# Kernel tuning notes

Hardware: AMD Instinct MI355X
Metric: run time of the kernel (lower is better)

## Reference

```python
import jax, jax.numpy as jnp
import numpy as np
from jax.ops import segment_sum

N, E, G, D, L = 50000, 800000, 1024, 300, 5
FEAT = 256
EPS = 1e-5


def setup_inputs() -> dict:
    key = jax.random.key(0)
    ks = jax.random.split(key, 20)
    x = jax.random.randint(ks[0], (N, 2), 0, 3)
    edge_index = jax.random.randint(ks[1], (2, E), 0, N)
    edge_attr = jax.random.randint(ks[2], (E, 2), 0, 3)
    batch = jnp.sort(jax.random.randint(ks[3], (N,), 0, G))
    s = 0.05
    x_emb1 = jax.random.normal(ks[4], (119, D), jnp.float32) * s
    x_emb2 = jax.random.normal(ks[5], (3, D), jnp.float32) * s
    W = jax.random.normal(ks[6], (L, D, D), jnp.float32) * (1.0 / np.sqrt(D))
    b = jnp.zeros((L, D), jnp.float32)
    e1 = jax.random.normal(ks[7], (L, 5, 1), jnp.float32) * s
    e2 = jax.random.normal(ks[8], (L, 3, 1), jnp.float32) * s
    gamma = jnp.ones((L, D), jnp.float32)
    beta = jnp.zeros((L, D), jnp.float32)
    feat_w = jax.random.normal(ks[9], (D, FEAT), jnp.float32) * (1.0 / np.sqrt(D))
    feat_b = jnp.zeros((FEAT,), jnp.float32)
    w1 = jax.random.normal(ks[10], (FEAT, FEAT), jnp.float32) * (1.0 / np.sqrt(FEAT))
    b1 = jnp.zeros((FEAT,), jnp.float32)
    w2 = jax.random.normal(ks[11], (FEAT, FEAT // 2), jnp.float32) * (1.0 / np.sqrt(FEAT))
    b2 = jnp.zeros((FEAT // 2,), jnp.float32)
    return dict(x=x, edge_index=edge_index, edge_attr=edge_attr, batch=batch,
                x_emb1=x_emb1, x_emb2=x_emb2, W=W, b=b, e1=e1, e2=e2,
                gamma=gamma, beta=beta, feat_w=feat_w, feat_b=feat_b,
                w1=w1, b1=b1, w2=w2, b2=b2)


def reference(x, edge_index, edge_attr, batch, x_emb1, x_emb2, W, b, e1, e2,
              gamma, beta, feat_w, feat_b, w1, b1, w2, b2):
    row, col = edge_index[0], edge_index[1]
    # node embedding: atom type + chirality
    h = x_emb1[x[:, 0]] + x_emb2[x[:, 1]]  # [N,D]
    for l in range(L):
        hw = h @ W[l]  # [N,D]
        # scalar edge embedding per edge (emb dim is 1 in the source)
        eemb = e1[l, edge_attr[:, 0], 0] + e2[l, edge_attr[:, 1], 0]  # [E]
        msg = hw[row] + eemb[:, None]  # [E,D]
        agg = segment_sum(msg, col, num_segments=N)
        # self loops: edge_attr = (4, 0)
        self_e = e1[l, 4, 0] + e2[l, 0, 0]
        h = agg + hw + self_e + b[l]
        # BatchNorm1d over nodes (batch statistics, biased var)
        mu = jnp.mean(h, axis=0)
        var = jnp.mean((h - mu) ** 2, axis=0)
        h = (h - mu) * jax.lax.rsqrt(var + EPS) * gamma[l] + beta[l]
        if l < L - 1:
            h = jax.nn.relu(h)
    # global mean pool per graph
    sums = segment_sum(h, batch, num_segments=G)  # [G,D]
    cnt = segment_sum(jnp.ones((h.shape[0],), h.dtype), batch, num_segments=G)
    hg = sums / jnp.maximum(cnt, 1.0)[:, None]
    h_feat = hg @ feat_w + feat_b  # [G,FEAT]
    out = jax.nn.relu(h_feat @ w1 + b1) @ w2 + b2  # [G,FEAT//2]
    return (h_feat, out)
```

## Files before the change

### kernel.cpp

```cpp
#include <hip/hip_runtime.h>
#include <hip/hip_bf16.h>

#define NN 50000
#define EE 800000
#define GG 1024
#define DD 300
#define DP 320
#define LL 5
#define FEAT 256

#define AGGB 6272

typedef __bf16 bf16x8 __attribute__((ext_vector_type(8)));
typedef float  f32x4  __attribute__((ext_vector_type(4)));

#define AS1 __attribute__((address_space(1)))
#define AS3 __attribute__((address_space(3)))

__device__ __forceinline__ void dma16(const __hip_bfloat16* g, __hip_bfloat16* l) {
    auto gp = reinterpret_cast<const AS1 char*>(reinterpret_cast<uintptr_t>(g));
    auto lp = reinterpret_cast<AS3 char*>((unsigned int)(uintptr_t)l);
    __builtin_amdgcn_global_load_lds(gp, lp, 16, 0, 0);
}

__device__ __forceinline__ void addbf8(float* a, int4 q) {
    unsigned int u;
    u = (unsigned int)q.x;
    a[0] += __uint_as_float(u << 16); a[1] += __uint_as_float(u & 0xFFFF0000u);
    u = (unsigned int)q.y;
    a[2] += __uint_as_float(u << 16); a[3] += __uint_as_float(u & 0xFFFF0000u);
    u = (unsigned int)q.z;
    a[4] += __uint_as_float(u << 16); a[5] += __uint_as_float(u & 0xFFFF0000u);
    u = (unsigned int)q.w;
    a[6] += __uint_as_float(u << 16); a[7] += __uint_as_float(u & 0xFFFF0000u);
}

__global__ void embed_kernel(const int* __restrict__ x,
                             const float* __restrict__ emb1,
                             const float* __restrict__ emb2,
                             __hip_bfloat16* __restrict__ A) {
    int idx = blockIdx.x * 256 + threadIdx.x;
    int v = idx / DP, d = idx % DP;
    float val = 0.f;
    if (d < DD) {
        int i0 = x[v * 2 + 0], i1 = x[v * 2 + 1];
        val = emb1[i0 * DD + d] + emb2[i1 * DD + d];
    }
    A[idx] = __float2bfloat16(val);
}

__global__ void hist_kernel(const int* __restrict__ ei, int* __restrict__ deg) {
    int e = blockIdx.x * 256 + threadIdx.x;
    atomicAdd(&deg[ei[EE + e]], 1);
}

__global__ void scan1_kernel(const int* __restrict__ deg, int* __restrict__ ptr,
                             int* __restrict__ bsum) {
    __shared__ int buf[256];
    int tid = threadIdx.x;
    int i = blockIdx.x * 256 + tid;
    int v = (i < NN) ? deg[i] : 0;
    buf[tid] = v; __syncthreads();
    for (int off = 1; off < 256; off <<= 1) {
        int t = (tid >= off) ? buf[tid - off] : 0;
        __syncthreads();
        buf[tid] += t;
        __syncthreads();
    }
    if (i < NN) ptr[i + 1] = buf[tid];
    if (tid == 255) bsum[blockIdx.x] = buf[255];
}

__global__ void scan2_kernel(int* __restrict__ bsum) {
    __shared__ int buf[256];
    int tid = threadIdx.x;
    int v = (tid < 196) ? bsum[tid] : 0;
    buf[tid] = v; __syncthreads();
    for (int off = 1; off < 256; off <<= 1) {
        int t = (tid >= off) ? buf[tid - off] : 0;
        __syncthreads();
        buf[tid] += t;
        __syncthreads();
    }
    if (tid < 196) bsum[tid] = buf[tid] - v;
}

__global__ void scan3_kernel(int* __restrict__ ptr, const int* __restrict__ bsum) {
    int i = blockIdx.x * 256 + threadIdx.x;
    if (i < NN) ptr[i + 1] += bsum[blockIdx.x];
    if (i == 0) ptr[0] = 0;
}

__global__ void scatter_kernel(const int* __restrict__ ei, const int* __restrict__ ea,
                               const int* __restrict__ ptr, int* __restrict__ cur,
                               int* __restrict__ srcout) {
    int e = blockIdx.x * 256 + threadIdx.x;
    int r = ei[e], c = ei[EE + e];
    int a0 = ea[e * 2 + 0], a1 = ea[e * 2 + 1];
    int pos = ptr[c] + atomicAdd(&cur[c], 1);
    srcout[pos] = r | (a0 << 16) | (a1 << 18);
}

__global__ void sv_kernel(const int* __restrict__ ptr, const int* __restrict__ src,
                          const float* __restrict__ e1, const float* __restrict__ e2,
                          float* __restrict__ SV) {
    int v = blockIdx.x * 256 + threadIdx.x;
    if (v >= NN) return;
    float c00 = 0.f, c01 = 0.f, c02 = 0.f, c10 = 0.f, c11 = 0.f, c12 = 0.f;
    int beg = ptr[v], end = ptr[v + 1];
    for (int i = beg; i < end; ++i) {
        int p = src[i];
        int e0 = (p >> 16) & 3, ev = (p >> 18) & 3;
        c00 += (e0 == 0); c01 += (e0 == 1); c02 += (e0 == 2);
        c10 += (ev == 0); c11 += (ev == 1); c12 += (ev == 2);
    }
#pragma unroll
    for (int l = 0; l < LL; ++l) {
        float s = c00 * e1[l * 5 + 0] + c01 * e1[l * 5 + 1] + c02 * e1[l * 5 + 2]
                + c10 * e2[l * 3 + 0] + c11 * e2[l * 3 + 1] + c12 * e2[l * 3 + 2];
        SV[l * NN + v] = s;
    }
}

__global__ void repack_kernel(const float* __restrict__ W,
                              __hip_bfloat16* __restrict__ WT) {
    int idx = blockIdx.x * 256 + threadIdx.x;
    int l = idx / (DP * DP);
    int r = idx - l * DP * DP;
    int ntile = r / 51200; r -= ntile * 51200;
    int ktile = r / 10240; r -= ktile * 10240;
    int nn = r >> 6; r &= 63;
    int pu = r >> 3; int e = r & 7;
    int u = pu ^ (nn & 7);
    int n = ntile * 160 + nn;
    int k = ktile * 64 + u * 8 + e;
    float v = 0.f;
    if (n < DD && k < DD) v = W[l * DD * DD + k * DD + n];
    WT[idx] = __float2bfloat16(v);
}

__global__ __launch_bounds__(256) void gemm_kernel(
        const __hip_bfloat16* __restrict__ A, const __hip_bfloat16* __restrict__ BT,
        __hip_bfloat16* __restrict__ C, int M,
        const float* __restrict__ scale, const float* __restrict__ shift, int fold) {
    __shared__ __align__(16) char smem[38912];
    __hip_bfloat16* As = reinterpret_cast<__hip_bfloat16*>(smem);
    __hip_bfloat16* Bs = reinterpret_cast<__hip_bfloat16*>(smem + 18432);
    __hip_bfloat16* Cs = reinterpret_cast<__hip_bfloat16*>(smem);
    int tid = threadIdx.x;
    int m0 = blockIdx.x * 128;
    int wave = tid >> 6, lane = tid & 63;
    int wm = (wave >> 1) * 64, wn = (wave & 1) * 80;
    int fm = lane & 15, fu = lane >> 4;

    f32x4 acc[4][5];
#pragma unroll
    for (int i = 0; i < 4; ++i)
#pragma unroll
        for (int j = 0; j < 5; ++j) acc[i][j] = (f32x4){0.f, 0.f, 0.f, 0.f};

    const __hip_bfloat16* btile0 = BT + (size_t)blockIdx.y * 51200;

    for (int k0 = 0; k0 < DP; k0 += 64) {
        __syncthreads();
        const __hip_bfloat16* bt = btile0 + (k0 >> 6) * 10240;
#pragma unroll
        for (int i = 0; i < 5; ++i)
            dma16(bt + (size_t)(tid + i * 256) * 8, Bs + (tid + i * 256) * 8);
#pragma unroll
        for (int u = tid; u < 1024; u += 256) {
            int r = u >> 3, p = u & 7;
            int gr = m0 + r;
            int4 val = make_int4(0, 0, 0, 0);
            if (gr < M) {
                val = *reinterpret_cast<const int4*>(A + (size_t)gr * DP + k0 + p * 8);
                if (fold) {
                    __hip_bfloat16* hh = reinterpret_cast<__hip_bfloat16*>(&val);
                    int kb = k0 + p * 8;
#pragma unroll
                    for (int j = 0; j < 8; ++j) {
                        float f = fmaf(__bfloat162float(hh[j]), scale[kb + j], shift[kb + j]);
                        hh[j] = __float2bfloat16(fmaxf(f, 0.f));
                    }
                }
            }
            *reinterpret_cast<int4*>(As + r * 72 + p * 8) = val;
        }
        __syncthreads();
#pragma unroll
        for (int h = 0; h < 2; ++h) {
            bf16x8 af[4], bfr[5];
#pragma unroll
            for (int mt = 0; mt < 4; ++mt)
                af[mt] = *reinterpret_cast<const bf16x8*>(
                    As + (wm + mt * 16 + fm) * 72 + h * 32 + fu * 8);
#pragma unroll
            for (int nt = 0; nt < 5; ++nt) {
                int n = wn + nt * 16 + fm;
                int pu = (h * 4 + fu) ^ (n & 7);
                bfr[nt] = *reinterpret_cast<const bf16x8*>(Bs + n * 64 + pu * 8);
            }
#pragma unroll
            for (int mt = 0; mt < 4; ++mt)
#pragma unroll
                for (int nt = 0; nt < 5; ++nt)
                    acc[mt][nt] = __builtin_amdgcn_mfma_f32_16x16x32_bf16(
                        af[mt], bfr[nt], acc[mt][nt], 0, 0, 0);
        }
    }
    int n0 = blockIdx.y * 160;
    int cc = lane & 15, cr = (lane >> 4) * 4;
#pragma unroll
    for (int h = 0; h < 2; ++h) {
        __syncthreads();
        if ((wave >> 1) == h) {
#pragma unroll
            for (int mt = 0; mt < 4; ++mt)
#pragma unroll
                for (int nt = 0; nt < 5; ++nt)
#pragma unroll
                    for (int r = 0; r < 4; ++r)
                        Cs[(mt * 16 + cr + r) * 168 + wn + nt * 16 + cc] =
                            __float2bfloat16(acc[mt][nt][r]);
        }
        __syncthreads();
#pragma unroll
        for (int u = tid; u < 1280; u += 256) {
            int r = u / 20, c16 = u % 20;
            int row = m0 + h * 64 + r;
            if (row < M)
                *reinterpret_cast<int4*>(C + (size_t)row * DP + n0 + c16 * 8) =
                    *reinterpret_cast<const int4*>(Cs + r * 168 + c16 * 8);
        }
    }
}

__global__ __launch_bounds__(256) void agg_kernel(
        const __hip_bfloat16* __restrict__ HW,
        const int* __restrict__ ptr, const int* __restrict__ src,
        const float* __restrict__ SVl, __hip_bfloat16* __restrict__ AH,
        float* __restrict__ part) {
    int w = threadIdx.x >> 6;
    int lane = threadIdx.x & 63;
    float sx = 0.f, sy = 0.f, sz = 0.f, sw = 0.f, st = 0.f;
    float qx = 0.f, qy = 0.f, qz = 0.f, qw = 0.f, qt = 0.f;

#pragma unroll
    for (int k = 0; k < 2; ++k) {
        int v = blockIdx.x * 8 + w * 2 + k;
        if (v >= NN) break;
        int beg = ptr[v], end = ptr[v + 1];
        const __hip_bfloat16* rv = HW + (size_t)v * DP;
        ushort4 qs = *reinterpret_cast<const ushort4*>(rv + 4 * lane);
        unsigned int ts = reinterpret_cast<const unsigned short*>(rv)[256 + lane];
        float A0x = __uint_as_float((unsigned int)qs.x << 16);
        float A0y = __uint_as_float((unsigned int)qs.y << 16);
        float A0z = __uint_as_float((unsigned int)qs.z << 16);
        float A0w = __uint_as_float((unsigned int)qs.w << 16);
        float A0t = __uint_as_float(ts << 16);
        float A1x = 0.f, A1y = 0.f, A1z = 0.f, A1w = 0.f, A1t = 0.f;
        float A2x = 0.f, A2y = 0.f, A2z = 0.f, A2w = 0.f, A2t = 0.f;
        float A3x = 0.f, A3y = 0.f, A3z = 0.f, A3w = 0.f, A3t = 0.f;
        int i = beg;
        for (; i < end && (i & 3); ++i) {
            int s0 = src[i] & 0xFFFF;
            const __hip_bfloat16* r0 = HW + (size_t)s0 * DP;
            ushort4 q0 = *reinterpret_cast<const ushort4*>(r0 + 4 * lane);
            unsigned int t0 = reinterpret_cast<const unsigned short*>(r0)[256 + lane];
            A0x += __uint_as_float((unsigned int)q0.x << 16);
            A0y += __uint_as_float((unsigned int)q0.y << 16);
            A0z += __uint_as_float((unsigned int)q0.z << 16);
            A0w += __uint_as_float((unsigned int)q0.w << 16);
            A0t += __uint_as_float(t0 << 16);
        }
        for (; i + 4 <= end; i += 4) {
            int4 s4 = *reinterpret_cast<const int4*>(src + i);
            int s0 = s4.x & 0xFFFF, s1 = s4.y & 0xFFFF;
            int s2 = s4.z & 0xFFFF, s3 = s4.w & 0xFFFF;
            const __hip_bfloat16* r0 = HW + (size_t)s0 * DP;
            const __hip_bfloat16* r1 = HW + (size_t)s1 * DP;
            const __hip_bfloat16* r2 = HW + (size_t)s2 * DP;
            const __hip_bfloat16* r3 = HW + (size_t)s3 * DP;
            ushort4 q0 = *reinterpret_cast<const ushort4*>(r0 + 4 * lane);
            ushort4 q1 = *reinterpret_cast<const ushort4*>(r1 + 4 * lane);
            ushort4 q2 = *reinterpret_cast<const ushort4*>(r2 + 4 * lane);
            ushort4 q3 = *reinterpret_cast<const ushort4*>(r3 + 4 * lane);
            unsigned int t0 = reinterpret_cast<const unsigned short*>(r0)[256 + lane];
            unsigned int t1 = reinterpret_cast<const unsigned short*>(r1)[256 + lane];
            unsigned int t2 = reinterpret_cast<const unsigned short*>(r2)[256 + lane];
            unsigned int t3 = reinterpret_cast<const unsigned short*>(r3)[256 + lane];
            A0x += __uint_as_float((unsigned int)q0.x << 16);
            A0y += __uint_as_float((unsigned int)q0.y << 16);
            A0z += __uint_as_float((unsigned int)q0.z << 16);
            A0w += __uint_as_float((unsigned int)q0.w << 16);
            A0t += __uint_as_float(t0 << 16);
            A1x += __uint_as_float((unsigned int)q1.x << 16);
            A1y += __uint_as_float((unsigned int)q1.y << 16);
            A1z += __uint_as_float((unsigned int)q1.z << 16);
            A1w += __uint_as_float((unsigned int)q1.w << 16);
            A1t += __uint_as_float(t1 << 16);
            A2x += __uint_as_float((unsigned int)q2.x << 16);
            A2y += __uint_as_float((unsigned int)q2.y << 16);
            A2z += __uint_as_float((unsigned int)q2.z << 16);
            A2w += __uint_as_float((unsigned int)q2.w << 16);
            A2t += __uint_as_float(t2 << 16);
            A3x += __uint_as_float((unsigned int)q3.x << 16);
            A3y += __uint_as_float((unsigned int)q3.y << 16);
            A3z += __uint_as_float((unsigned int)q3.z << 16);
            A3w += __uint_as_float((unsigned int)q3.w << 16);
            A3t += __uint_as_float(t3 << 16);
        }
        for (; i < end; ++i) {
            int s0 = src[i] & 0xFFFF;
            const __hip_bfloat16* r0 = HW + (size_t)s0 * DP;
            ushort4 q0 = *reinterpret_cast<const ushort4*>(r0 + 4 * lane);
            unsigned int t0 = reinterpret_cast<const unsigned short*>(r0)[256 + lane];
            A0x += __uint_as_float((unsigned int)q0.x << 16);
            A0y += __uint_as_float((unsigned int)q0.y << 16);
            A0z += __uint_as_float((unsigned int)q0.z << 16);
            A0w += __uint_as_float((unsigned int)q0.w << 16);
            A0t += __uint_as_float(t0 << 16);
        }
        float sv = SVl[v];
        float rx = A0x + A1x + A2x + A3x + sv;
        float ry = A0y + A1y + A2y + A3y + sv;
        float rz = A0z + A1z + A2z + A3z + sv;
        float rw = A0w + A1w + A2w + A3w + sv;
        float rt = A0t + A1t + A2t + A3t + sv;
        sx += rx; qx = fmaf(rx, rx, qx);
        sy += ry; qy = fmaf(ry, ry, qy);
        sz += rz; qz = fmaf(rz, rz, qz);
        sw += rw; qw = fmaf(rw, rw, qw);
        st += rt; qt = fmaf(rt, rt, qt);
        __hip_bfloat16* out = AH + (size_t)v * DP;
        union { ushort4 u; __hip_bfloat16 h[4]; } o;
        o.h[0] = __float2bfloat16(rx); o.h[1] = __float2bfloat16(ry);
        o.h[2] = __float2bfloat16(rz); o.h[3] = __float2bfloat16(rw);
        *reinterpret_cast<ushort4*>(out + 4 * lane) = o.u;
        out[256 + lane] = __float2bfloat16(lane < 44 ? rt : 0.f);
    }
    __shared__ float red[4 * 640];
    float* rw_ = red + w * 640;
    rw_[4 * lane + 0] = sx; rw_[4 * lane + 1] = sy;
    rw_[4 * lane + 2] = sz; rw_[4 * lane + 3] = sw;
    rw_[256 + lane] = (lane < 44) ? st : 0.f;
    rw_[320 + 4 * lane + 0] = qx; rw_[320 + 4 * lane + 1] = qy;
    rw_[320 + 4 * lane + 2] = qz; rw_[320 + 4 * lane + 3] = qw;
    rw_[320 + 256 + lane] = (lane < 44) ? qt : 0.f;
    __syncthreads();
    for (int i = threadIdx.x; i < 640; i += 256)
        part[(size_t)blockIdx.x * 640 + i] =
            red[i] + red[640 + i] + red[1280 + i] + red[1920 + i];
}

__global__ void finalize1_kernel(const float* __restrict__ part, float* __restrict__ part2) {
    int b = blockIdx.x;
    const int K = AGGB / 64;
    for (int i = threadIdx.x; i < 640; i += 256) {
        float acc = 0.f;
        for (int k = 0; k < K; ++k)
            acc += part[(size_t)(b * K + k) * 640 + i];
        part2[b * 640 + i] = acc;
    }
}

__global__ void finalize_kernel(const float* __restrict__ part2,
                                const float* __restrict__ gamma_l,
                                const float* __restrict__ beta_l,
                                float* __restrict__ scale, float* __restrict__ shift) {
    int d = threadIdx.x;
    float sc = 0.f, sh = 0.f;
    if (d < DD) {
        float s = 0.f, q = 0.f;
        for (int b = 0; b < 64; ++b) {
            s += part2[b * 640 + d];
            q += part2[b * 640 + 320 + d];
        }
        const float invN = 1.0f / (float)NN;
        float mean = s * invN;
        float var = q * invN - mean * mean;
        var = fmaxf(var, 0.f);
        float rs = rsqrtf(var + 1e-5f);
        sc = rs * gamma_l[d];
        sh = beta_l[d] - mean * sc;
    }
    scale[d] = sc;
    shift[d] = sh;
}

__device__ __forceinline__ int lower_bound_dev(const int* b, int n, int key) {
    int lo = 0, hi = n;
    while (lo < hi) { int mid = (lo + hi) >> 1; if (b[mid] < key) lo = mid + 1; else hi = mid; }
    return lo;
}

__global__ void pool_kernel(const __hip_bfloat16* __restrict__ A, const int* __restrict__ batch,
                            const float* __restrict__ scale, const float* __restrict__ shift,
                            float* __restrict__ HG) {
    int g = blockIdx.x * 4 + (threadIdx.x >> 6);
    int lane = threadIdx.x & 63;
    bool act = lane < 40;
    int lo = lower_bound_dev(batch, NN, g);
    int hi = lower_bound_dev(batch, NN, g + 1);
    const int4 z4 = make_int4(0, 0, 0, 0);
    float a[8];
#pragma unroll
    for (int j = 0; j < 8; ++j) a[j] = 0.f;
    for (int v = lo; v < hi; ++v) {
        int4 q = act ? *reinterpret_cast<const int4*>(A + (size_t)v * DP + 8 * lane) : z4;
        addbf8(a, q);
    }
    if (act) {
        int cnt = hi - lo;
        float inv = 1.0f / (float)(cnt > 0 ? cnt : 1);
        float* out = HG + (size_t)g * DP;
#pragma unroll
        for (int j = 0; j < 8; ++j) {
            int d = 8 * lane + j;
            out[d] = fmaf(a[j] * inv, scale[d], shift[d]);
        }
    }
}

__global__ void feat_kernel(const float* __restrict__ HG,
                            const float* __restrict__ fw,
                            const float* __restrict__ fb,
                            float* __restrict__ HFEAT, float* __restrict__ out0) {
    __shared__ float hgs[DD];
    int g = blockIdx.x, tid = threadIdx.x;
    for (int i = tid; i < DD; i += 256) hgs[i] = HG[(size_t)g * DP + i];
    __syncthreads();
    float acc = fb[tid];
#pragma unroll 4
    for (int k = 0; k < DD; ++k)
        acc = fmaf(hgs[k], fw[k * FEAT + tid], acc);
    HFEAT[g * FEAT + tid] = acc;
    out0[g * FEAT + tid] = acc;
}

__global__ void mlp_kernel(const float* __restrict__ HFEAT,
                           const float* __restrict__ w1, const float* __restrict__ b1,
                           const float* __restrict__ w2, const float* __restrict__ b2,
                           float* __restrict__ out1) {
    __shared__ float hf[FEAT], t[FEAT];
    int g = blockIdx.x, tid = threadIdx.x;
    hf[tid] = HFEAT[g * FEAT + tid];
    __syncthreads();
    float acc = b1[tid];
#pragma unroll 4
    for (int k = 0; k < FEAT; ++k)
        acc = fmaf(hf[k], w1[k * FEAT + tid], acc);
    t[tid] = fmaxf(acc, 0.f);
    __syncthreads();
    if (tid < FEAT / 2) {
        float acc2 = b2[tid];
#pragma unroll 4
        for (int k = 0; k < FEAT; ++k)
            acc2 = fmaf(t[k], w2[k * (FEAT / 2) + tid], acc2);
        out1[g * (FEAT / 2) + tid] = acc2;
    }
}

extern "C" void kernel_launch(void* const* d_in, const int* in_sizes, int n_in,
                              void* d_out, int out_size, void* d_ws, size_t ws_size,
                              hipStream_t stream) {
    const int* x     = (const int*)d_in[0];
    const int* ei    = (const int*)d_in[1];
    const int* ea    = (const int*)d_in[2];
    const int* batch = (const int*)d_in[3];
    const float* emb1  = (const float*)d_in[4];
    const float* emb2  = (const float*)d_in[5];
    const float* W     = (const float*)d_in[6];
    const float* e1    = (const float*)d_in[8];
    const float* e2    = (const float*)d_in[9];
    const float* gamma = (const float*)d_in[10];
    const float* beta  = (const float*)d_in[11];
    const float* fw    = (const float*)d_in[12];
    const float* fb    = (const float*)d_in[13];
    const float* w1    = (const float*)d_in[14];
    const float* b1    = (const float*)d_in[15];
    const float* w2    = (const float*)d_in[16];
    const float* b2    = (const float*)d_in[17];

    char* base = (char*)d_ws;
    size_t off = 0;
    auto carve = [&](size_t bytes) -> void* {
        void* p = base + off;
        off = (off + bytes + 255) & ~(size_t)255;
        return p;
    };
    int*            PTR   = (int*)carve((size_t)(NN + 1) * 4);
    int*            CUR   = (int*)carve((size_t)NN * 4);
    int*            SRC   = (int*)carve((size_t)EE * 4);
    float*          SV    = (float*)carve((size_t)LL * NN * 4);
    int*            BSUM  = (int*)carve(256 * 4);
    float*          PART  = (float*)carve((size_t)AGGB * 640 * 4);
    float*          PART2 = (float*)carve((size_t)64 * 640 * 4);
    float*          SCALE = (float*)carve(DP * 4);
    float*          SHIFT = (float*)carve(DP * 4);
    float*          HG    = (float*)carve((size_t)GG * DP * 4);
    float*          HFEAT = (float*)carve((size_t)GG * FEAT * 4);
    __hip_bfloat16* WT    = (__hip_bfloat16*)carve((size_t)LL * DP * DP * 2);
    __hip_bfloat16* AH    = (__hip_bfloat16*)carve((size_t)NN * DP * 2);
    __hip_bfloat16* HWb   = (__hip_bfloat16*)carve((size_t)NN * DP * 2);

    float* out0 = (float*)d_out;
    float* out1 = (float*)d_out + GG * FEAT;

    hipMemsetAsync(CUR, 0, (size_t)NN * 4, stream);
    embed_kernel<<<(NN * DP) / 256, 256, 0, stream>>>(x, emb1, emb2, AH);
    hist_kernel<<<EE / 256, 256, 0, stream>>>(ei, CUR);
    scan1_kernel<<<196, 256, 0, stream>>>(CUR, PTR, BSUM);
    scan2_kernel<<<1, 256, 0, stream>>>(BSUM);
    scan3_kernel<<<196, 256, 0, stream>>>(PTR, BSUM);
    hipMemsetAsync(CUR, 0, (size_t)NN * 4, stream);
    scatter_kernel<<<EE / 256, 256, 0, stream>>>(ei, ea, PTR, CUR, SRC);
    sv_kernel<<<196, 256, 0, stream>>>(PTR, SRC, e1, e2, SV);
    repack_kernel<<<(LL * DP * DP) / 256, 256, 0, stream>>>(W, WT);

    for (int l = 0; l < LL; ++l) {
        gemm_kernel<<<dim3(391, 2), 256, 0, stream>>>(AH, WT + (size_t)l * DP * DP, HWb, NN,
                                                      SCALE, SHIFT, l > 0 ? 1 : 0);
        agg_kernel<<<AGGB, 256, 0, stream>>>(HWb, PTR, SRC, SV + (size_t)l * NN, AH, PART);
        finalize1_kernel<<<64, 256, 0, stream>>>(PART, PART2);
        finalize_kernel<<<1, 320, 0, stream>>>(PART2, gamma + l * DD, beta + l * DD, SCALE, SHIFT);
    }

    pool_kernel<<<GG / 4, 256, 0, stream>>>(AH, batch, SCALE, SHIFT, HG);
    feat_kernel<<<GG, 256, 0, stream>>>(HG, fw, fb, HFEAT, out0);
    mlp_kernel<<<GG, 256, 0, stream>>>(HFEAT, w1, b1, w2, b2, out1);
}
```

Before: 958.0 us.

## Restructure GEMM to 64-row full-width tiles with per-wave N slices and direct A loads

```diff
diff --git a/kernel.cpp b/kernel.cpp
--- a/kernel.cpp
+++ b/kernel.cpp
@@ -9,9 +9,10 @@
 #define LL 5
 #define FEAT 256
 
-#define AGGB 6272
+#define AGGB 3136
 
 typedef __bf16 bf16x8 __attribute__((ext_vector_type(8)));
+typedef unsigned short u16x8 __attribute__((ext_vector_type(8)));
 typedef float  f32x4  __attribute__((ext_vector_type(4)));
 
 #define AS1 __attribute__((address_space(1)))
@@ -21,6 +22,10 @@
     auto gp = reinterpret_cast<const AS1 char*>(reinterpret_cast<uintptr_t>(g));
     auto lp = reinterpret_cast<AS3 char*>((unsigned int)(uintptr_t)l);
     __builtin_amdgcn_global_load_lds(gp, lp, 16, 0, 0);
+}
+
+__device__ __forceinline__ float bf2f(unsigned short u) {
+    return __uint_as_float((unsigned int)u << 16);
 }
 
 __device__ __forceinline__ void addbf8(float* a, int4 q) {
@@ -127,12 +132,12 @@
     int idx = blockIdx.x * 256 + threadIdx.x;
     int l = idx / (DP * DP);
     int r = idx - l * DP * DP;
-    int ntile = r / 51200; r -= ntile * 51200;
-    int ktile = r / 10240; r -= ktile * 10240;
+    int nt = r / 25600;    r -= nt * 25600;
+    int ktile = r / 5120;  r -= ktile * 5120;
     int nn = r >> 6; r &= 63;
     int pu = r >> 3; int e = r & 7;
     int u = pu ^ (nn & 7);
-    int n = ntile * 160 + nn;
+    int n = nt * 80 + nn;
     int k = ktile * 64 + u * 8 + e;
     float v = 0.f;
     if (n < DD && k < DD) v = W[l * DD * DD + k * DD + n];
@@ -143,14 +148,12 @@
         const __hip_bfloat16* __restrict__ A, const __hip_bfloat16* __restrict__ BT,
         __hip_bfloat16* __restrict__ C, int M,
         const float* __restrict__ scale, const float* __restrict__ shift, int fold) {
-    __shared__ __align__(16) char smem[38912];
-    __hip_bfloat16* As = reinterpret_cast<__hip_bfloat16*>(smem);
-    __hip_bfloat16* Bs = reinterpret_cast<__hip_bfloat16*>(smem + 18432);
+    __shared__ __align__(16) char smem[41984];
+    __hip_bfloat16* Bs = reinterpret_cast<__hip_bfloat16*>(smem);
     __hip_bfloat16* Cs = reinterpret_cast<__hip_bfloat16*>(smem);
     int tid = threadIdx.x;
-    int m0 = blockIdx.x * 128;
+    int m0 = blockIdx.x * 64;
     int wave = tid >> 6, lane = tid & 63;
-    int wm = (wave >> 1) * 64, wn = (wave & 1) * 80;
     int fm = lane & 15, fu = lane >> 4;
 
     f32x4 acc[4][5];
@@ -159,79 +162,90 @@
 #pragma unroll
         for (int j = 0; j < 5; ++j) acc[i][j] = (f32x4){0.f, 0.f, 0.f, 0.f};
 
-    const __hip_bfloat16* btile0 = BT + (size_t)blockIdx.y * 51200;
-
-    for (int k0 = 0; k0 < DP; k0 += 64) {
-        __syncthreads();
-        const __hip_bfloat16* bt = btile0 + (k0 >> 6) * 10240;
-#pragma unroll
-        for (int i = 0; i < 5; ++i)
-            dma16(bt + (size_t)(tid + i * 256) * 8, Bs + (tid + i * 256) * 8);
-#pragma unroll
-        for (int u = tid; u < 1024; u += 256) {
-            int r = u >> 3, p = u & 7;
-            int gr = m0 + r;
-            int4 val = make_int4(0, 0, 0, 0);
-            if (gr < M) {
-                val = *reinterpret_cast<const int4*>(A + (size_t)gr * DP + k0 + p * 8);
-                if (fold) {
-                    __hip_bfloat16* hh = reinterpret_cast<__hip_bfloat16*>(&val);
-                    int kb = k0 + p * 8;
+    const __hip_bfloat16* bbase = BT + (size_t)wave * 25600;
+    __hip_bfloat16* bs = Bs + wave * 5120;
+
+    for (int kt = 0; kt < 5; ++kt) {
+        int k0 = kt * 64;
+        const __hip_bfloat16* bt = bbase + kt * 5120;
+#pragma unroll
+        for (int j = 0; j < 10; ++j)
+            dma16(bt + (size_t)(lane + j * 64) * 8, bs + (lane + j * 64) * 8);
+        u16x8 af[2][4];
+#pragma unroll
+        for (int h = 0; h < 2; ++h) {
+#pragma unroll
+            for (int mt = 0; mt < 4; ++mt) {
+                int row = m0 + mt * 16 + fm;
+                int kb = k0 + h * 32 + fu * 8;
+                u16x8 v = (u16x8)(short)0;
+                if (row < M)
+                    v = *reinterpret_cast<const u16x8*>(A + (size_t)row * DP + kb);
+                af[h][mt] = v;
+            }
+        }
+        __builtin_amdgcn_s_waitcnt(0);
+        __builtin_amdgcn_sched_barrier(0);
+        if (fold) {
+#pragma unroll
+            for (int h = 0; h < 2; ++h) {
+                int kb = k0 + h * 32 + fu * 8;
+                float4 s0 = *reinterpret_cast<const float4*>(scale + kb);
+                float4 s1 = *reinterpret_cast<const float4*>(scale + kb + 4);
+                float4 t0 = *reinterpret_cast<const float4*>(shift + kb);
+                float4 t1 = *reinterpret_cast<const float4*>(shift + kb + 4);
+                float ss[8] = {s0.x, s0.y, s0.z, s0.w, s1.x, s1.y, s1.z, s1.w};
+                float tt[8] = {t0.x, t0.y, t0.z, t0.w, t1.x, t1.y, t1.z, t1.w};
+#pragma unroll
+                for (int mt = 0; mt < 4; ++mt) {
+                    union { u16x8 v; __hip_bfloat16 hh[8]; } o;
+                    o.v = af[h][mt];
 #pragma unroll
                     for (int j = 0; j < 8; ++j) {
-                        float f = fmaf(__bfloat162float(hh[j]), scale[kb + j], shift[kb + j]);
-                        hh[j] = __float2bfloat16(fmaxf(f, 0.f));
+                        float f = fmaf(bf2f(((unsigned short*)&o.v)[j]), ss[j], tt[j]);
+                        o.hh[j] = __float2bfloat16(fmaxf(f, 0.f));
                     }
+                    af[h][mt] = o.v;
                 }
             }
-            *reinterpret_cast<int4*>(As + r * 72 + p * 8) = val;
-        }
-        __syncthreads();
+        }
 #pragma unroll
         for (int h = 0; h < 2; ++h) {
-            bf16x8 af[4], bfr[5];
-#pragma unroll
-            for (int mt = 0; mt < 4; ++mt)
-                af[mt] = *reinterpret_cast<const bf16x8*>(
-                    As + (wm + mt * 16 + fm) * 72 + h * 32 + fu * 8);
+            bf16x8 bfr[5];
 #pragma unroll
             for (int nt = 0; nt < 5; ++nt) {
-                int n = wn + nt * 16 + fm;
-                int pu = (h * 4 + fu) ^ (n & 7);
-                bfr[nt] = *reinterpret_cast<const bf16x8*>(Bs + n * 64 + pu * 8);
+                int nl = nt * 16 + fm;
+                bfr[nt] = *reinterpret_cast<const bf16x8*>(
+                    bs + nl * 64 + (((h * 4 + fu) ^ (nl & 7)) * 8));
             }
 #pragma unroll
             for (int mt = 0; mt < 4; ++mt)
 #pragma unroll
                 for (int nt = 0; nt < 5; ++nt)
                     acc[mt][nt] = __builtin_amdgcn_mfma_f32_16x16x32_bf16(
-                        af[mt], bfr[nt], acc[mt][nt], 0, 0, 0);
-        }
-    }
-    int n0 = blockIdx.y * 160;
+                        *reinterpret_cast<bf16x8*>(&af[h][mt]), bfr[nt],
+                        acc[mt][nt], 0, 0, 0);
+        }
+        __builtin_amdgcn_sched_barrier(0);
+    }
     int cc = lane & 15, cr = (lane >> 4) * 4;
-#pragma unroll
-    for (int h = 0; h < 2; ++h) {
-        __syncthreads();
-        if ((wave >> 1) == h) {
-#pragma unroll
-            for (int mt = 0; mt < 4; ++mt)
-#pragma unroll
-                for (int nt = 0; nt < 5; ++nt)
-#pragma unroll
-                    for (int r = 0; r < 4; ++r)
-                        Cs[(mt * 16 + cr + r) * 168 + wn + nt * 16 + cc] =
-                            __float2bfloat16(acc[mt][nt][r]);
-        }
-        __syncthreads();
-#pragma unroll
-        for (int u = tid; u < 1280; u += 256) {
-            int r = u / 20, c16 = u % 20;
-            int row = m0 + h * 64 + r;
-            if (row < M)
-                *reinterpret_cast<int4*>(C + (size_t)row * DP + n0 + c16 * 8) =
-                    *reinterpret_cast<const int4*>(Cs + r * 168 + c16 * 8);
-        }
+    __syncthreads();
+#pragma unroll
+    for (int mt = 0; mt < 4; ++mt)
+#pragma unroll
+        for (int nt = 0; nt < 5; ++nt)
+#pragma unroll
+            for (int r = 0; r < 4; ++r)
+                Cs[(mt * 16 + cr + r) * 328 + wave * 80 + nt * 16 + cc] =
+                    __float2bfloat16(acc[mt][nt][r]);
+    __syncthreads();
+#pragma unroll
+    for (int u = tid; u < 2560; u += 256) {
+        int r = u / 40, c16 = u % 40;
+        int row = m0 + r;
+        if (row < M)
+            *reinterpret_cast<int4*>(C + (size_t)row * DP + c16 * 8) =
+                *reinterpret_cast<const int4*>(Cs + r * 328 + c16 * 8);
     }
 }
 
@@ -246,8 +260,8 @@
     float qx = 0.f, qy = 0.f, qz = 0.f, qw = 0.f, qt = 0.f;
 
 #pragma unroll
-    for (int k = 0; k < 2; ++k) {
-        int v = blockIdx.x * 8 + w * 2 + k;
+    for (int k = 0; k < 4; ++k) {
+        int v = blockIdx.x * 16 + w * 4 + k;
         if (v >= NN) break;
         int beg = ptr[v], end = ptr[v + 1];
         const __hip_bfloat16* rv = HW + (size_t)v * DP;
@@ -519,8 +533,8 @@
     repack_kernel<<<(LL * DP * DP) / 256, 256, 0, stream>>>(W, WT);
 
     for (int l = 0; l < LL; ++l) {
-        gemm_kernel<<<dim3(391, 2), 256, 0, stream>>>(AH, WT + (size_t)l * DP * DP, HWb, NN,
-                                                      SCALE, SHIFT, l > 0 ? 1 : 0);
+        gemm_kernel<<<782, 256, 0, stream>>>(AH, WT + (size_t)l * DP * DP, HWb, NN,
+                                             SCALE, SHIFT, l > 0 ? 1 : 0);
         agg_kernel<<<AGGB, 256, 0, stream>>>(HWb, PTR, SRC, SV + (size_t)l * NN, AH, PART);
         finalize1_kernel<<<64, 256, 0, stream>>>(PART, PART2);
         finalize_kernel<<<1, 320, 0, stream>>>(PART2, gamma + l * DD, beta + l * DD, SCALE, SHIFT);
```

Result: slower. 986.3 us (+3.0%).
